# Kernel optimization log

Hardware: AMD Instinct MI355X
Metric: run time of the kernel (lower is better)

Reference implementation:

```python
import jax, jax.numpy as jnp
import numpy as np

B, N, D = 2, 1024, 128
H = D // 2  # edge_importance hidden width


def setup_inputs() -> dict:
    key = jax.random.key(0)
    k0, k1, k2, k3, k4 = jax.random.split(key, 5)
    node_embeddings = jax.random.normal(k0, (B, N, D), dtype=jnp.float32)
    visited = jax.random.randint(k1, (B, N), 0, 2).astype(bool)
    remaining_capacity = jax.random.uniform(k2, (B, 1), dtype=jnp.float32)
    # edge_importance: Linear(2D -> H) -> ReLU -> Linear(H -> 1)
    W1 = jax.random.normal(k3, (H, 2 * D), dtype=jnp.float32) / np.sqrt(2 * D)
    b1 = jnp.zeros((H,), dtype=jnp.float32)
    W2 = jax.random.normal(k4, (1, H), dtype=jnp.float32) / np.sqrt(H)
    b2 = jnp.zeros((1,), dtype=jnp.float32)
    return {"node_embeddings": node_embeddings, "visited": visited,
            "remaining_capacity": remaining_capacity,
            "W1": W1, "b1": b1, "W2": W2, "b2": b2}


def reference(node_embeddings, visited, remaining_capacity, W1, b1, W2, b2):
    d = node_embeddings.shape[-1]
    # Linear on concat([node_i, node_j]) == split-weight sum; avoids the
    # [B,N,N,2D] concat while computing identical math.
    Wi, Wj = W1[:, :d], W1[:, d:]
    ai = jnp.einsum('bnd,hd->bnh', node_embeddings, Wi)  # [B,N,H]
    aj = jnp.einsum('bnd,hd->bnh', node_embeddings, Wj)  # [B,N,H]
    hidden = jax.nn.relu(ai[:, :, None, :] + aj[:, None, :, :] + b1)  # [B,N,N,H]
    edge_weights = jnp.einsum('bijh,oh->bij', hidden, W2) + b2[0]      # [B,N,N]
    visited_mask = visited[:, None, :] | visited[:, :, None]           # [B,N,N]
    edge_weights = jnp.where(visited_mask, jnp.float32(-1e9), edge_weights)
    adjacency = jax.nn.softmax(edge_weights, axis=-1)
    return adjacency
```

## Files before the change

kernel.cpp:

```cpp
#include <hip/hip_runtime.h>

#define Bb 2
#define Nn 1024
#define Dd 128
#define Hh 64

__global__ __launch_bounds__(256)
void k1_proj(const float* __restrict__ E, const float* __restrict__ W1,
             const float* __restrict__ b1, float* __restrict__ Pt,
             float* __restrict__ Qt) {
  __shared__ float El[64 * 129];
  __shared__ float Wl[128 * 33];

  const int t = threadIdx.x;
  const int oBase = blockIdx.x * 32;
  const int nBase = blockIdx.y * 64;
  const int b = blockIdx.z;

  const float* esrc = E + ((size_t)b * Nn + nBase) * Dd;
  #pragma unroll
  for (int k = 0; k < 8; ++k) {
    int q = t + k * 256;
    int n = q >> 5;
    int c = (q & 31) << 2;
    float4 v = *(const float4*)(esrc + n * Dd + c);
    float* dst = &El[n * 129 + c];
    dst[0] = v.x; dst[1] = v.y; dst[2] = v.z; dst[3] = v.w;
  }
  #pragma unroll
  for (int k = 0; k < 16; ++k) {
    int q = t + k * 256;
    int o = q >> 7;
    int d = q & 127;
    int oG = oBase + o;
    int src = (oG < Hh) ? (oG * 2 * Dd + d) : ((oG - Hh) * 2 * Dd + Dd + d);
    Wl[d * 33 + o] = W1[src];
  }
  __syncthreads();

  const int tn = t & 15;
  const int to = t >> 4;
  float acc[4][2] = {{0.f, 0.f}, {0.f, 0.f}, {0.f, 0.f}, {0.f, 0.f}};
  #pragma unroll 8
  for (int d = 0; d < 128; ++d) {
    float w0 = Wl[d * 33 + to * 2 + 0];
    float w1 = Wl[d * 33 + to * 2 + 1];
    #pragma unroll
    for (int a = 0; a < 4; ++a) {
      float e = El[(tn * 4 + a) * 129 + d];
      acc[a][0] = fmaf(e, w0, acc[a][0]);
      acc[a][1] = fmaf(e, w1, acc[a][1]);
    }
  }

  #pragma unroll
  for (int j = 0; j < 2; ++j) {
    int o = oBase + to * 2 + j;
    float4 v = make_float4(acc[0][j], acc[1][j], acc[2][j], acc[3][j]);
    float* dst;
    if (o < Hh) {
      float bias = b1[o];
      v.x += bias; v.y += bias; v.z += bias; v.w += bias;
      dst = Pt + ((size_t)b * Hh + o) * Nn + nBase + tn * 4;
    } else {
      dst = Qt + ((size_t)b * Hh + (o - Hh)) * Nn + nBase + tn * 4;
    }
    *(float4*)dst = v;
  }
}

__global__ __launch_bounds__(256)
void k2_edge(const float* __restrict__ Pt, const float* __restrict__ Qt,
             const float* __restrict__ W2, const float* __restrict__ b2,
             float* __restrict__ edge) {
  __shared__ float Pl[64 * 68];
  __shared__ float Ql[64 * 68];

  const int t = threadIdx.x;
  const int jBase = blockIdx.x * 64;
  const int iBase = blockIdx.y * 64;
  const int b = blockIdx.z;

  #pragma unroll
  for (int k = 0; k < 4; ++k) {
    int q = t + k * 256;
    int h = q >> 4;
    int c = (q & 15) << 2;
    float4 pv = *(const float4*)(Pt + ((size_t)b * Hh + h) * Nn + iBase + c);
    *(float4*)&Pl[h * 68 + c] = pv;
    float4 qv = *(const float4*)(Qt + ((size_t)b * Hh + h) * Nn + jBase + c);
    *(float4*)&Ql[h * 68 + c] = qv;
  }
  __syncthreads();

  const int tx = t & 15;
  const int ty = t >> 4;
  float acc[4][4] = {};
  #pragma unroll 4
  for (int h = 0; h < 64; ++h) {
    float w = W2[h];
    float4 pv = *(const float4*)&Pl[h * 68 + ty * 4];
    float4 qv = *(const float4*)&Ql[h * 68 + tx * 4];
    float p[4]  = {pv.x, pv.y, pv.z, pv.w};
    float qa[4] = {qv.x, qv.y, qv.z, qv.w};
    #pragma unroll
    for (int a = 0; a < 4; ++a)
      #pragma unroll
      for (int c = 0; c < 4; ++c)
        acc[a][c] = fmaf(w, fmaxf(p[a] + qa[c], 0.f), acc[a][c]);
  }

  const float b2v = b2[0];
  float* erow = edge + ((size_t)b * Nn + iBase + ty * 4) * Nn + jBase + tx * 4;
  #pragma unroll
  for (int a = 0; a < 4; ++a) {
    float4 v = make_float4(acc[a][0] + b2v, acc[a][1] + b2v,
                           acc[a][2] + b2v, acc[a][3] + b2v);
    *(float4*)(erow + (size_t)a * Nn) = v;
  }
}

__global__ __launch_bounds__(256)
void k3_softmax(float* __restrict__ out, const int* __restrict__ visited) {
  const int r = blockIdx.x;
  const int b = r >> 10;
  const int t = threadIdx.x;
  __shared__ float redm[4];
  __shared__ float reds[4];

  const bool vi = visited[r] != 0;
  float* row = out + (size_t)r * Nn;
  const int4 vj = *(const int4*)(visited + b * Nn + t * 4);
  const float4 ev = *(const float4*)(row + t * 4);

  const float NEG = -1000000000.0f;
  float v0 = (vi | (vj.x != 0)) ? NEG : ev.x;
  float v1 = (vi | (vj.y != 0)) ? NEG : ev.y;
  float v2 = (vi | (vj.z != 0)) ? NEG : ev.z;
  float v3 = (vi | (vj.w != 0)) ? NEG : ev.w;

  float m = fmaxf(fmaxf(v0, v1), fmaxf(v2, v3));
  #pragma unroll
  for (int off = 32; off > 0; off >>= 1)
    m = fmaxf(m, __shfl_xor(m, off));
  if ((t & 63) == 0) redm[t >> 6] = m;
  __syncthreads();
  m = fmaxf(fmaxf(redm[0], redm[1]), fmaxf(redm[2], redm[3]));

  float e0 = __expf(v0 - m), e1 = __expf(v1 - m);
  float e2 = __expf(v2 - m), e3 = __expf(v3 - m);
  float s = (e0 + e1) + (e2 + e3);
  #pragma unroll
  for (int off = 32; off > 0; off >>= 1)
    s += __shfl_xor(s, off);
  if ((t & 63) == 0) reds[t >> 6] = s;
  __syncthreads();
  s = (reds[0] + reds[1]) + (reds[2] + reds[3]);

  const float inv = 1.0f / s;
  *(float4*)(row + t * 4) = make_float4(e0 * inv, e1 * inv, e2 * inv, e3 * inv);
}

extern "C" void kernel_launch(void* const* d_in, const int* in_sizes, int n_in,
                              void* d_out, int out_size, void* d_ws, size_t ws_size,
                              hipStream_t stream) {
  const float* E       = (const float*)d_in[0];
  const int*   visited = (const int*)d_in[1];
  const float* W1      = (const float*)d_in[3];
  const float* b1      = (const float*)d_in[4];
  const float* W2      = (const float*)d_in[5];
  const float* b2      = (const float*)d_in[6];

  float* out = (float*)d_out;
  float* Pt  = (float*)d_ws;
  float* Qt  = (float*)((char*)d_ws + (size_t)Bb * Hh * Nn * sizeof(float));

  k1_proj<<<dim3(4, 16, Bb), 256, 0, stream>>>(E, W1, b1, Pt, Qt);
  k2_edge<<<dim3(16, 16, Bb), 256, 0, stream>>>(Pt, Qt, W2, b2, out);
  k3_softmax<<<dim3(Bb * Nn), 256, 0, stream>>>(out, visited);
}
```

Measured before the change: 91.68 us.

## Fuse edge scoring and masked softmax into one kernel with async LDS staging

Merges the edge MLP kernel and the softmax kernel, so each block computes full rows (8 rows per block, 2 per wavefront) in registers and applies the mask and softmax before writing. This removes the write and re-read of the B*N*N edge tensor and one kernel launch. Q is streamed in double-buffered chunks via global_load_lds. The tradeoff is lower reuse of P and Q per block (each Q element is reused by only 8 rows), only 256 blocks, and more registers per thread, which could limit occupancy.

```diff
diff --git a/kernel.cpp b/kernel.cpp
--- a/kernel.cpp
+++ b/kernel.cpp
@@ -4,6 +4,9 @@
 #define Nn 1024
 #define Dd 128
 #define Hh 64
+#define CHUNK 256
+#define NCHUNK (Nn / CHUNK)
+#define IT 8
 
 __global__ __launch_bounds__(256)
 void k1_proj(const float* __restrict__ E, const float* __restrict__ W1,
@@ -69,96 +72,126 @@
   }
 }
 
+__device__ __forceinline__ void gload_lds16(const float* g, float* l) {
+  __builtin_amdgcn_global_load_lds(
+      (const __attribute__((address_space(1))) void*)g,
+      (__attribute__((address_space(3))) void*)l, 16, 0, 0);
+}
+
 __global__ __launch_bounds__(256)
-void k2_edge(const float* __restrict__ Pt, const float* __restrict__ Qt,
-             const float* __restrict__ W2, const float* __restrict__ b2,
-             float* __restrict__ edge) {
-  __shared__ float Pl[64 * 68];
-  __shared__ float Ql[64 * 68];
-
-  const int t = threadIdx.x;
-  const int jBase = blockIdx.x * 64;
-  const int iBase = blockIdx.y * 64;
-  const int b = blockIdx.z;
-
-  #pragma unroll
-  for (int k = 0; k < 4; ++k) {
-    int q = t + k * 256;
-    int h = q >> 4;
-    int c = (q & 15) << 2;
-    float4 pv = *(const float4*)(Pt + ((size_t)b * Hh + h) * Nn + iBase + c);
-    *(float4*)&Pl[h * 68 + c] = pv;
-    float4 qv = *(const float4*)(Qt + ((size_t)b * Hh + h) * Nn + jBase + c);
-    *(float4*)&Ql[h * 68 + c] = qv;
-  }
+void k23_fused(const float* __restrict__ Pt, const float* __restrict__ Qt,
+               const float* __restrict__ W2, const float* __restrict__ b2,
+               const int* __restrict__ visited, float* __restrict__ out) {
+  __shared__ float Ql[2][Hh][CHUNK];
+  __shared__ float Pl[Hh][IT];
+
+  const int t  = threadIdx.x;
+  const int tx = t & 63;
+  const int ty = t >> 6;
+  const int iBase = blockIdx.x * IT;
+  const int b  = blockIdx.y;
+
+  #pragma unroll
+  for (int k = 0; k < 2; ++k) {
+    int e = t + k * 256;
+    int h = e >> 3, i = e & 7;
+    Pl[h][i] = Pt[((size_t)b * Hh + h) * Nn + iBase + i];
+  }
+
+  const float* qb = Qt + (size_t)b * Hh * Nn;
+
+  auto stage = [&](int buf, int ch) {
+    const int jB = ch * CHUNK;
+    #pragma unroll
+    for (int r = 0; r < 16; ++r) {
+      const int h = ty * 16 + r;
+      gload_lds16(qb + (size_t)h * Nn + jB + tx * 4, &Ql[buf][h][0]);
+    }
+  };
+
+  float acc[2][16];
+  #pragma unroll
+  for (int k = 0; k < 16; ++k) { acc[0][k] = 0.f; acc[1][k] = 0.f; }
+
+  stage(0, 0);
   __syncthreads();
 
-  const int tx = t & 15;
-  const int ty = t >> 4;
-  float acc[4][4] = {};
-  #pragma unroll 4
-  for (int h = 0; h < 64; ++h) {
-    float w = W2[h];
-    float4 pv = *(const float4*)&Pl[h * 68 + ty * 4];
-    float4 qv = *(const float4*)&Ql[h * 68 + tx * 4];
-    float p[4]  = {pv.x, pv.y, pv.z, pv.w};
-    float qa[4] = {qv.x, qv.y, qv.z, qv.w};
+  #pragma unroll
+  for (int ch = 0; ch < NCHUNK; ++ch) {
+    const int buf = ch & 1;
+    if (ch + 1 < NCHUNK) stage(buf ^ 1, ch + 1);
+
+    #pragma unroll 8
+    for (int h = 0; h < Hh; ++h) {
+      const float  w = W2[h];
+      const float4 q = *(const float4*)&Ql[buf][h][tx * 4];
+      const float p0 = Pl[h][2 * ty + 0];
+      const float p1 = Pl[h][2 * ty + 1];
+      const float qa[4] = {q.x, q.y, q.z, q.w};
+      #pragma unroll
+      for (int c = 0; c < 4; ++c) {
+        acc[0][ch * 4 + c] = fmaf(w, fmaxf(p0 + qa[c], 0.f), acc[0][ch * 4 + c]);
+        acc[1][ch * 4 + c] = fmaf(w, fmaxf(p1 + qa[c], 0.f), acc[1][ch * 4 + c]);
+      }
+    }
+    __syncthreads();
+  }
+
+  const float NEG = -1000000000.0f;
+  const float b2v = b2[0];
+  const int vrow = b * Nn;
+  const bool vi0 = visited[vrow + iBase + 2 * ty + 0] != 0;
+  const bool vi1 = visited[vrow + iBase + 2 * ty + 1] != 0;
+
+  float m0 = NEG, m1 = NEG;
+  #pragma unroll
+  for (int ch = 0; ch < NCHUNK; ++ch) {
+    const int4 vj = *(const int4*)(visited + vrow + ch * CHUNK + tx * 4);
+    const int vja[4] = {vj.x, vj.y, vj.z, vj.w};
     #pragma unroll
-    for (int a = 0; a < 4; ++a)
-      #pragma unroll
-      for (int c = 0; c < 4; ++c)
-        acc[a][c] = fmaf(w, fmaxf(p[a] + qa[c], 0.f), acc[a][c]);
-  }
-
-  const float b2v = b2[0];
-  float* erow = edge + ((size_t)b * Nn + iBase + ty * 4) * Nn + jBase + tx * 4;
-  #pragma unroll
-  for (int a = 0; a < 4; ++a) {
-    float4 v = make_float4(acc[a][0] + b2v, acc[a][1] + b2v,
-                           acc[a][2] + b2v, acc[a][3] + b2v);
-    *(float4*)(erow + (size_t)a * Nn) = v;
-  }
-}
-
-__global__ __launch_bounds__(256)
-void k3_softmax(float* __restrict__ out, const int* __restrict__ visited) {
-  const int r = blockIdx.x;
-  const int b = r >> 10;
-  const int t = threadIdx.x;
-  __shared__ float redm[4];
-  __shared__ float reds[4];
-
-  const bool vi = visited[r] != 0;
-  float* row = out + (size_t)r * Nn;
-  const int4 vj = *(const int4*)(visited + b * Nn + t * 4);
-  const float4 ev = *(const float4*)(row + t * 4);
-
-  const float NEG = -1000000000.0f;
-  float v0 = (vi | (vj.x != 0)) ? NEG : ev.x;
-  float v1 = (vi | (vj.y != 0)) ? NEG : ev.y;
-  float v2 = (vi | (vj.z != 0)) ? NEG : ev.z;
-  float v3 = (vi | (vj.w != 0)) ? NEG : ev.w;
-
-  float m = fmaxf(fmaxf(v0, v1), fmaxf(v2, v3));
-  #pragma unroll
-  for (int off = 32; off > 0; off >>= 1)
-    m = fmaxf(m, __shfl_xor(m, off));
-  if ((t & 63) == 0) redm[t >> 6] = m;
-  __syncthreads();
-  m = fmaxf(fmaxf(redm[0], redm[1]), fmaxf(redm[2], redm[3]));
-
-  float e0 = __expf(v0 - m), e1 = __expf(v1 - m);
-  float e2 = __expf(v2 - m), e3 = __expf(v3 - m);
-  float s = (e0 + e1) + (e2 + e3);
-  #pragma unroll
-  for (int off = 32; off > 0; off >>= 1)
-    s += __shfl_xor(s, off);
-  if ((t & 63) == 0) reds[t >> 6] = s;
-  __syncthreads();
-  s = (reds[0] + reds[1]) + (reds[2] + reds[3]);
-
-  const float inv = 1.0f / s;
-  *(float4*)(row + t * 4) = make_float4(e0 * inv, e1 * inv, e2 * inv, e3 * inv);
+    for (int c = 0; c < 4; ++c) {
+      const bool mj = vja[c] != 0;
+      float v0 = (vi0 | mj) ? NEG : (acc[0][ch * 4 + c] + b2v);
+      float v1 = (vi1 | mj) ? NEG : (acc[1][ch * 4 + c] + b2v);
+      acc[0][ch * 4 + c] = v0;
+      acc[1][ch * 4 + c] = v1;
+      m0 = fmaxf(m0, v0);
+      m1 = fmaxf(m1, v1);
+    }
+  }
+  #pragma unroll
+  for (int off = 32; off; off >>= 1) {
+    m0 = fmaxf(m0, __shfl_xor(m0, off));
+    m1 = fmaxf(m1, __shfl_xor(m1, off));
+  }
+
+  float s0 = 0.f, s1 = 0.f;
+  #pragma unroll
+  for (int k = 0; k < 16; ++k) {
+    const float e0 = __expf(acc[0][k] - m0);
+    const float e1 = __expf(acc[1][k] - m1);
+    acc[0][k] = e0; acc[1][k] = e1;
+    s0 += e0; s1 += e1;
+  }
+  #pragma unroll
+  for (int off = 32; off; off >>= 1) {
+    s0 += __shfl_xor(s0, off);
+    s1 += __shfl_xor(s1, off);
+  }
+  const float i0 = 1.0f / s0, i1 = 1.0f / s1;
+
+  float* o0 = out + (size_t)(b * Nn + iBase + 2 * ty + 0) * Nn;
+  float* o1 = out + (size_t)(b * Nn + iBase + 2 * ty + 1) * Nn;
+  #pragma unroll
+  for (int ch = 0; ch < NCHUNK; ++ch) {
+    const int j = ch * CHUNK + tx * 4;
+    float4 w0 = make_float4(acc[0][ch * 4 + 0] * i0, acc[0][ch * 4 + 1] * i0,
+                            acc[0][ch * 4 + 2] * i0, acc[0][ch * 4 + 3] * i0);
+    float4 w1 = make_float4(acc[1][ch * 4 + 0] * i1, acc[1][ch * 4 + 1] * i1,
+                            acc[1][ch * 4 + 2] * i1, acc[1][ch * 4 + 3] * i1);
+    *(float4*)(o0 + j) = w0;
+    *(float4*)(o1 + j) = w1;
+  }
 }
 
 extern "C" void kernel_launch(void* const* d_in, const int* in_sizes, int n_in,
@@ -176,6 +209,5 @@
   float* Qt  = (float*)((char*)d_ws + (size_t)Bb * Hh * Nn * sizeof(float));
 
   k1_proj<<<dim3(4, 16, Bb), 256, 0, stream>>>(E, W1, b1, Pt, Qt);
-  k2_edge<<<dim3(16, 16, Bb), 256, 0, stream>>>(Pt, Qt, W2, b2, out);
-  k3_softmax<<<dim3(Bb * Nn), 256, 0, stream>>>(out, visited);
-}
+  k23_fused<<<dim3(Nn / IT, Bb), 256, 0, stream>>>(Pt, Qt, W2, b2, visited, out);
+}
```

Result: slower. 94.71 us (+3.3%).
